# Kernel tuning notes

Measured on AMD Instinct MI355X. Metric: run time of the kernel, lower is better.

Reference implementation:

```python
import jax, jax.numpy as jnp
import numpy as np

BN_EPS = 1e-5
THRESH = 0.81


def _prelu(x, w):
    return jnp.where(x >= 0, x, w * x)


def setup_inputs() -> dict:
    key = jax.random.key(0)
    k1, = jax.random.split(key, 1)
    B, F, L = 8, 2048, 1024
    x = jax.random.normal(k1, (B, F, L), dtype=jnp.float32)
    # PReLU weights (default num_parameters=1, init=0.25)
    prelu1_w = jnp.full((1,), 0.25, dtype=jnp.float32)
    prelu2_w = jnp.full((1,), 0.25, dtype=jnp.float32)
    # BatchNorm1d(nfeat) affine params (default init weight=1, bias=0)
    bn_weight = jnp.ones((F,), dtype=jnp.float32)
    bn_bias = jnp.zeros((F,), dtype=jnp.float32)
    return {"x": x, "prelu1_w": prelu1_w, "prelu2_w": prelu2_w,
            "bn_weight": bn_weight, "bn_bias": bn_bias}


def reference(x, prelu1_w, prelu2_w, bn_weight, bn_bias):
    # x: [B, F, L]
    B, F, L = x.shape
    # --- Adj_Dynamic: PReLU -> AdaptiveAvgPool1d(1) -> BatchNorm1d (training-mode batch stats)
    h = _prelu(x, prelu1_w)                       # [B, F, L]
    h = jnp.mean(h, axis=-1, keepdims=True)       # [B, F, 1]
    mu = jnp.mean(h, axis=(0, 2), keepdims=True)  # per-channel mean over (B, L=1)
    var = jnp.mean((h - mu) ** 2, axis=(0, 2), keepdims=True)  # biased variance
    h = (h - mu) * jax.lax.rsqrt(var + BN_EPS)
    h = h * bn_weight[None, :, None] + bn_bias[None, :, None]  # [B, F, 1]
    # --- dynamic adjacency
    sim = jnp.einsum('bni,bmi->bnm', h, h)        # [B, F, F]
    I = jnp.eye(F, dtype=x.dtype)
    A = jnp.where(sim > THRESH, 1.0, 0.0) + I     # [B, F, F]
    # --- symmetric degree normalization D^-1/2 A D^-1/2 (diag matmuls as row/col scaling)
    d_inv_sqrt = jnp.sum(A, axis=-1) ** -0.5      # [B, F]
    A_hat = d_inv_sqrt[:, :, None] * A * d_inv_sqrt[:, None, :]
    # --- output PReLU
    return _prelu(A_hat, prelu2_w)
```

## Files before the change

kernel.cpp:

```cpp
#include <hip/hip_runtime.h>

#define B 8
#define F 2048
#define L 1024
#define BN_EPS 1e-5f
#define THRESH 0.81f

typedef float nt4 __attribute__((ext_vector_type(4)));

__global__ __launch_bounds__(256) void poolbn_kernel(const float* __restrict__ x,
                                                     const float* __restrict__ p1,
                                                     const float* __restrict__ bnw,
                                                     const float* __restrict__ bnb,
                                                     float* __restrict__ h) {
    __shared__ float hh[B];
    const int f    = blockIdx.x;
    const int wave = threadIdx.x >> 6;
    const int lane = threadIdx.x & 63;
    const float w  = p1[0];
#pragma unroll
    for (int b = wave; b < B; b += 4) {
        const nt4* xr = (const nt4*)(x + ((size_t)b * F + f) * L);
        float sum = 0.f;
#pragma unroll
        for (int k = 0; k < 4; ++k) {
            nt4 v = __builtin_nontemporal_load(&xr[lane + 64 * k]);
            sum += (v.x >= 0.f) ? v.x : w * v.x;
            sum += (v.y >= 0.f) ? v.y : w * v.y;
            sum += (v.z >= 0.f) ? v.z : w * v.z;
            sum += (v.w >= 0.f) ? v.w : w * v.w;
        }
#pragma unroll
        for (int off = 32; off > 0; off >>= 1)
            sum += __shfl_down(sum, off, 64);
        if (lane == 0) hh[b] = sum * (1.0f / L);
    }
    __syncthreads();
    if (threadIdx.x == 0) {
        float mu = 0.f;
#pragma unroll
        for (int b = 0; b < B; ++b) mu += hh[b];
        mu *= (1.0f / B);
        float var = 0.f;
#pragma unroll
        for (int b = 0; b < B; ++b) { float d = hh[b] - mu; var += d * d; }
        var *= (1.0f / B);
        const float scale = (1.0f / sqrtf(var + BN_EPS)) * bnw[f];
        const float bias  = bnb[f];
#pragma unroll
        for (int b = 0; b < B; ++b) h[b * F + f] = (hh[b] - mu) * scale + bias;
    }
}

__global__ __launch_bounds__(256) void deg_kernel(const float* __restrict__ hn,
                                                  float* __restrict__ dinv) {
    __shared__ float sh[F];
    __shared__ int partial[4][64];
    const int b    = blockIdx.x / (F / 64);
    const int nblk = blockIdx.x % (F / 64);
    for (int i = threadIdx.x; i < F; i += 256) sh[i] = hn[b * F + i];
    __syncthreads();
    const int nl = threadIdx.x & 63;
    const int q  = threadIdx.x >> 6;
    const int n  = nblk * 64 + nl;
    const float hv = sh[n];
    int cnt = 0;
    const int m0 = q * (F / 4);
    for (int m = 0; m < F / 4; m += 4) {
        float4 hm = *(const float4*)&sh[m0 + m];
        cnt += (hv * hm.x > THRESH);
        cnt += (hv * hm.y > THRESH);
        cnt += (hv * hm.z > THRESH);
        cnt += (hv * hm.w > THRESH);
    }
    partial[q][nl] = cnt;
    __syncthreads();
    if (q == 0) {
        int deg = 1 + partial[0][nl] + partial[1][nl] + partial[2][nl] + partial[3][nl];
        dinv[b * F + n] = 1.0f / sqrtf((float)deg);
    }
}

#define ROWS 8
__global__ __launch_bounds__(256) void out_kernel(const float* __restrict__ hn,
                                                  const float* __restrict__ dinv,
                                                  const float* __restrict__ p2,
                                                  float* __restrict__ out) {
    const int g  = blockIdx.x;
    const int b  = g / (F / ROWS);
    const int n0 = (g % (F / ROWS)) * ROWS;
    const float w2 = p2[0];
    const float* hrow = hn + b * F;
    const float* drow = dinv + b * F;
    float hv[ROWS], dn[ROWS];
#pragma unroll
    for (int r = 0; r < ROWS; ++r) { hv[r] = hrow[n0 + r]; dn[r] = drow[n0 + r]; }
    const float4* hm4 = (const float4*)hrow;
    const float4* dm4 = (const float4*)drow;
#pragma unroll
    for (int t = threadIdx.x; t < F / 4; t += 256) {
        float4 hm = hm4[t];
        float4 dm = dm4[t];
        const int m = t * 4;
#pragma unroll
        for (int r = 0; r < ROWS; ++r) {
            const int n = n0 + r;
            nt4 rr;
            {
                float a = (hv[r] * hm.x > THRESH) ? 1.f : 0.f; if (n == m + 0) a += 1.f;
                float v = (dn[r] * a) * dm.x; rr.x = (v >= 0.f) ? v : w2 * v;
            }
            {
                float a = (hv[r] * hm.y > THRESH) ? 1.f : 0.f; if (n == m + 1) a += 1.f;
                float v = (dn[r] * a) * dm.y; rr.y = (v >= 0.f) ? v : w2 * v;
            }
            {
                float a = (hv[r] * hm.z > THRESH) ? 1.f : 0.f; if (n == m + 2) a += 1.f;
                float v = (dn[r] * a) * dm.z; rr.z = (v >= 0.f) ? v : w2 * v;
            }
            {
                float a = (hv[r] * hm.w > THRESH) ? 1.f : 0.f; if (n == m + 3) a += 1.f;
                float v = (dn[r] * a) * dm.w; rr.w = (v >= 0.f) ? v : w2 * v;
            }
            __builtin_nontemporal_store(rr, (nt4*)(out + (size_t)(b * F + n) * F) + t);
        }
    }
}

extern "C" void kernel_launch(void* const* d_in, const int* in_sizes, int n_in,
                              void* d_out, int out_size, void* d_ws, size_t ws_size,
                              hipStream_t stream) {
    const float* x   = (const float*)d_in[0];
    const float* p1  = (const float*)d_in[1];
    const float* p2  = (const float*)d_in[2];
    const float* bnw = (const float*)d_in[3];
    const float* bnb = (const float*)d_in[4];
    float* out = (float*)d_out;

    float* h    = (float*)d_ws;
    float* dinv = h + B * F;

    poolbn_kernel<<<F, 256, 0, stream>>>(x, p1, bnw, bnb, h);
    deg_kernel<<<B * (F / 64), 256, 0, stream>>>(h, dinv);
    out_kernel<<<(B * F) / ROWS, 256, 0, stream>>>(h, dinv, p2, out);
}
```

Measured before the change: 195.1 us.

## Drop identity output PReLU, widen out kernel, split degree count finer

The output kernel now uses 512 threads so each thread handles exactly one float4 column per row. The final PReLU is removed because the normalized adjacency is always non-negative, which also removes a parameter load and several selects per element. The diagonal term is applied once per row, and the threshold result is fused directly into a select of the scaled value. The degree kernel uses 32-row blocks with 8 partial sums, doubling the block count for more parallelism. The pooling kernel switches from nontemporal to regular vector loads, which changes cache behaviour for the 64MB input read.

```diff
diff --git a/kernel.cpp b/kernel.cpp
--- a/kernel.cpp
+++ b/kernel.cpp
@@ -20,11 +20,11 @@
     const float w  = p1[0];
 #pragma unroll
     for (int b = wave; b < B; b += 4) {
-        const nt4* xr = (const nt4*)(x + ((size_t)b * F + f) * L);
+        const float4* xr = (const float4*)(x + ((size_t)b * F + f) * L);
         float sum = 0.f;
 #pragma unroll
         for (int k = 0; k < 4; ++k) {
-            nt4 v = __builtin_nontemporal_load(&xr[lane + 64 * k]);
+            float4 v = xr[lane + 64 * k];
             sum += (v.x >= 0.f) ? v.x : w * v.x;
             sum += (v.y >= 0.f) ? v.y : w * v.y;
             sum += (v.z >= 0.f) ? v.z : w * v.z;
@@ -55,18 +55,18 @@
 __global__ __launch_bounds__(256) void deg_kernel(const float* __restrict__ hn,
                                                   float* __restrict__ dinv) {
     __shared__ float sh[F];
-    __shared__ int partial[4][64];
-    const int b    = blockIdx.x / (F / 64);
-    const int nblk = blockIdx.x % (F / 64);
+    __shared__ int partial[8][32];
+    const int b    = blockIdx.x / (F / 32);
+    const int nblk = blockIdx.x % (F / 32);
     for (int i = threadIdx.x; i < F; i += 256) sh[i] = hn[b * F + i];
     __syncthreads();
-    const int nl = threadIdx.x & 63;
-    const int q  = threadIdx.x >> 6;
-    const int n  = nblk * 64 + nl;
+    const int nl = threadIdx.x & 31;
+    const int q  = threadIdx.x >> 5;
+    const int n  = nblk * 32 + nl;
     const float hv = sh[n];
     int cnt = 0;
-    const int m0 = q * (F / 4);
-    for (int m = 0; m < F / 4; m += 4) {
+    const int m0 = q * (F / 8);
+    for (int m = 0; m < F / 8; m += 4) {
         float4 hm = *(const float4*)&sh[m0 + m];
         cnt += (hv * hm.x > THRESH);
         cnt += (hv * hm.y > THRESH);
@@ -75,55 +75,44 @@
     }
     partial[q][nl] = cnt;
     __syncthreads();
-    if (q == 0) {
-        int deg = 1 + partial[0][nl] + partial[1][nl] + partial[2][nl] + partial[3][nl];
+    if (threadIdx.x < 32) {
+        int deg = 1;
+#pragma unroll
+        for (int qq = 0; qq < 8; ++qq) deg += partial[qq][nl];
         dinv[b * F + n] = 1.0f / sqrtf((float)deg);
     }
 }
 
 #define ROWS 8
-__global__ __launch_bounds__(256) void out_kernel(const float* __restrict__ hn,
+__global__ __launch_bounds__(512) void out_kernel(const float* __restrict__ hn,
                                                   const float* __restrict__ dinv,
-                                                  const float* __restrict__ p2,
                                                   float* __restrict__ out) {
     const int g  = blockIdx.x;
     const int b  = g / (F / ROWS);
     const int n0 = (g % (F / ROWS)) * ROWS;
-    const float w2 = p2[0];
+    const int t  = threadIdx.x;
     const float* hrow = hn + b * F;
     const float* drow = dinv + b * F;
     float hv[ROWS], dn[ROWS];
 #pragma unroll
     for (int r = 0; r < ROWS; ++r) { hv[r] = hrow[n0 + r]; dn[r] = drow[n0 + r]; }
-    const float4* hm4 = (const float4*)hrow;
-    const float4* dm4 = (const float4*)drow;
+    float4 hm = ((const float4*)hrow)[t];
+    float4 dm = ((const float4*)drow)[t];
+    float hma[4] = {hm.x, hm.y, hm.z, hm.w};
+    float dma[4] = {dm.x, dm.y, dm.z, dm.w};
+    const int td = n0 >> 2;
+    float* obase = out + ((size_t)(b * F + n0)) * F + 4 * t;
 #pragma unroll
-    for (int t = threadIdx.x; t < F / 4; t += 256) {
-        float4 hm = hm4[t];
-        float4 dm = dm4[t];
-        const int m = t * 4;
+    for (int r = 0; r < ROWS; ++r) {
+        const float hvr = hv[r];
+        const float s   = dn[r];
+        float va[4];
 #pragma unroll
-        for (int r = 0; r < ROWS; ++r) {
-            const int n = n0 + r;
-            nt4 rr;
-            {
-                float a = (hv[r] * hm.x > THRESH) ? 1.f : 0.f; if (n == m + 0) a += 1.f;
-                float v = (dn[r] * a) * dm.x; rr.x = (v >= 0.f) ? v : w2 * v;
-            }
-            {
-                float a = (hv[r] * hm.y > THRESH) ? 1.f : 0.f; if (n == m + 1) a += 1.f;
-                float v = (dn[r] * a) * dm.y; rr.y = (v >= 0.f) ? v : w2 * v;
-            }
-            {
-                float a = (hv[r] * hm.z > THRESH) ? 1.f : 0.f; if (n == m + 2) a += 1.f;
-                float v = (dn[r] * a) * dm.z; rr.z = (v >= 0.f) ? v : w2 * v;
-            }
-            {
-                float a = (hv[r] * hm.w > THRESH) ? 1.f : 0.f; if (n == m + 3) a += 1.f;
-                float v = (dn[r] * a) * dm.w; rr.w = (v >= 0.f) ? v : w2 * v;
-            }
-            __builtin_nontemporal_store(rr, (nt4*)(out + (size_t)(b * F + n) * F) + t);
-        }
+        for (int j = 0; j < 4; ++j)
+            va[j] = (hvr * hma[j] > THRESH) ? s * dma[j] : 0.f;
+        if (t == td + (r >> 2)) va[r & 3] += s * dma[r & 3];
+        nt4 rr = {va[0], va[1], va[2], va[3]};
+        __builtin_nontemporal_store(rr, (nt4*)(obase + (size_t)r * F));
     }
 }
 
@@ -132,7 +121,6 @@
                               hipStream_t stream) {
     const float* x   = (const float*)d_in[0];
     const float* p1  = (const float*)d_in[1];
-    const float* p2  = (const float*)d_in[2];
     const float* bnw = (const float*)d_in[3];
     const float* bnb = (const float*)d_in[4];
     float* out = (float*)d_out;
@@ -141,6 +129,6 @@
     float* dinv = h + B * F;
 
     poolbn_kernel<<<F, 256, 0, stream>>>(x, p1, bnw, bnb, h);
-    deg_kernel<<<B * (F / 64), 256, 0, stream>>>(h, dinv);
-    out_kernel<<<(B * F) / ROWS, 256, 0, stream>>>(h, dinv, p2, out);
+    deg_kernel<<<B * (F / 32), 256, 0, stream>>>(h, dinv);
+    out_kernel<<<(B * F) / ROWS, 512, 0, stream>>>(h, dinv, out);
 }
```

Result: no change. 197.4 us (+1.2%).
